# Performance work log

Measured on AMD Instinct MI355X. Metric: run time of the kernel, lower is better.

## Reference

```python
import jax, jax.numpy as jnp
import numpy as np

N, H, DK, DV, DFF, D = 2, 8, 32, 32, 512, 256
B, S = 2, 2048
MASK_VALUE = -1e-30
EPS = 1e-14  # K.epsilon()**2 with default epsilon 1e-7


def glorot(key, shape):
    fan_in, fan_out = shape[-2], shape[-1]
    limit = np.sqrt(6.0 / (fan_in + fan_out))
    return jax.random.uniform(key, shape, jnp.float32, -limit, limit)


def setup_inputs() -> dict:
    key = jax.random.key(0)
    ks = jax.random.split(key, 8)
    return {
        "x": jax.random.normal(ks[0], (B, S, D), jnp.float32),
        "mask": jnp.ones((B, S), jnp.float32),
        "Wq": glorot(ks[1], (N, H, D, DK)),
        "Wk": glorot(ks[2], (N, H, D, DK)),
        "Wv": glorot(ks[3], (N, H, D, DV)),
        "Wo": glorot(ks[4], (N, H * DV, D)),
        "W1": glorot(ks[5], (N, D, DFF)),
        "b1": jnp.zeros((N, DFF), jnp.float32),
        "W2": glorot(ks[6], (N, DFF, D)),
        "b2": jnp.zeros((N, D), jnp.float32),
        "gamma": jnp.ones((2 * N,), jnp.float32),
        "beta": jnp.zeros((2 * N,), jnp.float32),
    }


def _layernorm(x, g, b):
    mean = jnp.mean(x, axis=-1, keepdims=True)
    var = jnp.mean(jnp.square(x - mean), axis=-1, keepdims=True)
    return (x - mean) / jnp.sqrt(var + EPS) * g + b


def reference(x, mask, Wq, Wk, Wv, Wo, W1, b1, W2, b2, gamma, beta):
    m = mask[:, None, None, :]  # [B,1,1,S], multiplies score rows' key axis
    for i in range(N):
        # batched multi-head attention (no 1/sqrt(dk) scaling, faithful to source)
        q = jnp.einsum("bsd,hdk->bhsk", x, Wq[i])
        k = jnp.einsum("bsd,hdk->bhsk", x, Wk[i])
        v = jnp.einsum("bsd,hdv->bhsv", x, Wv[i])
        A = jnp.einsum("bhsk,bhtk->bhst", q, k)  # [B,H,S,S]
        A = m * A + (1.0 - m) * MASK_VALUE
        A = jax.nn.softmax(A, axis=-1)
        o = jnp.einsum("bhst,bhtv->bhsv", A, v)
        conc = o.transpose(0, 2, 1, 3).reshape(x.shape[0], x.shape[1], H * DV)
        x = x + conc @ Wo[i]
        x = _layernorm(x, gamma[2 * i], beta[2 * i])
        ffn = jax.nn.relu(x @ W1[i] + b1[i]) @ W2[i] + b2[i]
        x = x + ffn
        x = _layernorm(x, gamma[2 * i + 1], beta[2 * i + 1])
    return x
```

## Files before the change

### kernel.cpp

```cpp
#include <hip/hip_runtime.h>
#include <hip/hip_bf16.h>

#define NL 2
#define NH 8
#define DKk 32
#define DVv 32
#define DFF 512
#define DD 256
#define BB 2
#define SS 2048
#define MROWS (BB*SS)
#define LN_EPS 1e-14f
#define L2E 1.4426950408889634f
#define SOFT_SHIFT_L2E (50.0f*L2E)

typedef __hip_bfloat16 bf16;
typedef unsigned short us;
typedef short bf16x8 __attribute__((ext_vector_type(8)));
typedef float f32x4  __attribute__((ext_vector_type(4)));
typedef unsigned short us4 __attribute__((ext_vector_type(4)));

#define O_XF   256
#define O_QB   (O_XF+1048576)
#define O_KH   (O_QB+1048576)
#define O_KL   (O_KH+524288)
#define O_VT   (O_KL+524288)
#define O_XH   (O_VT+524288)
#define O_XL   (O_XH+524288)
#define O_OP   (O_XL+524288)
#define O_ML   (O_OP+2097152)
#define O_MASK (O_ML+65536)
#define O_B1   (O_MASK+4096)
#define O_B2   (O_B1+1024)
#define O_GM   (O_B2+512)
#define O_BT   (O_GM+4)
#define O_PREP (O_BT+4)
#define TAIL_TOTAL (4096+1024+512+4+4)
#define CONV_BLOCKS (512 + (TAIL_TOTAL+255)/256)
#define PREP_BLOCKS 512
#define PQH 0u
#define PQL 393216u
#define POH 786432u
#define POL 917504u
#define P1H 1048576u
#define P1L 1310720u
#define P2H 1572864u
#define P2L 1835008u

__device__ __forceinline__ float us2f(us u){
  unsigned int v = ((unsigned int)u) << 16; float f;
  __builtin_memcpy(&f, &v, 4); return f;
}
__device__ __forceinline__ us f2bf_rne(float f){
  unsigned int b = __float_as_uint(f);
  b += 0x7FFFu + ((b>>16)&1u);
  return (us)(b>>16);
}

#if __has_builtin(__builtin_amdgcn_exp2f)
#define EXP2F(x) __builtin_amdgcn_exp2f(x)
#else
#define EXP2F(x) exp2f(x)
#endif

#if __has_builtin(__builtin_amdgcn_cvt_pk_bf16_f32)
typedef __bf16 bf16x2_t __attribute__((ext_vector_type(2)));
__device__ __forceinline__ int pack_bf16(float a, float b){
  bf16x2_t r = __builtin_amdgcn_cvt_pk_bf16_f32(a, b);
  int i; __builtin_memcpy(&i, &r, 4); return i;
}
#else
__device__ __forceinline__ int pack_bf16(float a, float b){
  int b0 = __float_as_int(a) + 0x8000;
  int b1 = __float_as_int(b) + 0x8000;
  return (b1 & 0xFFFF0000) | ((int)((unsigned)b0 >> 16));
}
#endif

__device__ __forceinline__ f32x4 MF(bf16x8 a, bf16x8 b, f32x4 c){
  return __builtin_amdgcn_mfma_f32_16x16x32_bf16(a,b,c,0,0,0);
}

__device__ __forceinline__ void gl_lds16(const us* g, us* l){
  __builtin_amdgcn_global_load_lds(
    (const __attribute__((address_space(1))) unsigned int*)g,
    (__attribute__((address_space(3))) unsigned int*)l, 16, 0, 0);
}

__device__ __forceinline__ size_t xhl_idx(int row, int col){
  int rt = row>>6, rg = (row>>4)&3, L15 = row&15;
  int kc = col>>5, Q = (col>>3)&3, j = col&7;
  return ((size_t)(rt*8+kc))*2048 + rg*512 + Q*128 + L15*8 + j;
}

__device__ __forceinline__ float conv1(const void* src, size_t i, int flag){
  if(flag) return ((const float*)src)[i];
  return us2f(((const us*)src)[i]);
}

__device__ __forceinline__ void prep_b_raw(const void* W0, const void* W1v, const void* W2v,
                                           int baseoff, us* __restrict__ Bh, us* __restrict__ Bl,
                                           int Kd, int Nd, int qkv, int g, int flag)
{
  int total = (Kd/32)*(Nd/16)*64;
  if(g >= total) return;
  int lane = g & 63, fi = g >> 6;
  int ncN = Nd/16;
  int nc = fi % ncN, kc = fi / ncN;
  int Q = lane>>4, L15 = lane&15;
  int n = nc*16 + L15;
  const void* src;
  int off0, stride;
  if(qkv){
    int sec = n>>8, h = (n>>5)&7, kq = n&31;
    src = (sec==0)?W0:((sec==1)?W1v:W2v);
    off0 = baseoff + h*8192 + kq;
    stride = 32;
  } else {
    src = W0;
    off0 = baseoff + n;
    stride = Nd;
  }
  #pragma unroll
  for(int j=0;j<8;j++){
    int k = kc*32 + Q*8 + j;
    float v = conv1(src, (size_t)off0 + (size_t)k*stride, flag);
    us hb = f2bf_rne(v);
    Bh[(size_t)g*8 + j] = hb;
    Bl[(size_t)g*8 + j] = f2bf_rne(v - us2f(hb));
  }
}

__global__ void conv_prep(const void* s0, const void* s1, const void* sWq, const void* sWk,
                          const void* sWv, const void* sWo, const void* sW1, const void* sb1,
                          const void* sW2, const void* sb2, const void* sgm, const void* sbt,
                          float* __restrict__ ws, int* __restrict__ flagp)
{
  __shared__ int fsh[4];
  int bad = 0;
  const us* xr = (const us*)s0;
  for(int i=threadIdx.x; i<4096; i+=256){
    float f = us2f(xr[i]);
    if(!(fabsf(f) < 1e3f)) bad = 1;
  }
  unsigned long long m = __ballot(bad);
  if((threadIdx.x&63)==0) fsh[threadIdx.x>>6] = (m!=0ull);
  __syncthreads();
  int flag = (fsh[0]|fsh[1]|fsh[2]|fsh[3]);
  if(blockIdx.x==0 && threadIdx.x==0) *flagp = flag;

  int b = blockIdx.x;
  if(b < PREP_BLOCKS){
    int layer = b >> 8, lb = b & 255;
    us* prep = (us*)(ws + O_PREP);
    if(lb < 96){
      int g = lb*256 + threadIdx.x;
      prep_b_raw(sWq, sWk, sWv, layer*65536, prep+PQH+(size_t)layer*196608,
                 prep+PQL+(size_t)layer*196608, 256, 768, 1, g, flag);
    } else if(lb < 128){
      int g = (lb-96)*256 + threadIdx.x;
      prep_b_raw(sWo, nullptr, nullptr, layer*65536, prep+POH+(size_t)layer*65536,
                 prep+POL+(size_t)layer*65536, 256, 256, 0, g, flag);
    } else if(lb < 192){
      int g = (lb-128)*256 + threadIdx.x;
      prep_b_raw(sW1, nullptr, nullptr, layer*131072, prep+P1H+(size_t)layer*131072,
                 prep+P1L+(size_t)layer*131072, 256, 512, 0, g, flag);
    } else {
      int g = (lb-192)*256 + threadIdx.x;
      prep_b_raw(sW2, nullptr, nullptr, layer*131072, prep+P2H+(size_t)layer*131072,
                 prep+P2L+(size_t)layer*131072, 512, 256, 0, g, flag);
    }
    return;
  }
  int b2 = b - PREP_BLOCKS;
  if(b2 < 512){
    int g8 = b2*256 + threadIdx.x;
    int e0 = g8*8;
    float v[8];
    if(flag){
      float4 a0 = *((const float4*)s0 + (e0>>2));
      float4 a1 = *((const float4*)s0 + (e0>>2) + 1);
      v[0]=a0.x; v[1]=a0.y; v[2]=a0.z; v[3]=a0.w;
      v[4]=a1.x; v[5]=a1.y; v[6]=a1.z; v[7]=a1.w;
    } else {
      bf16x8 u = *((const bf16x8*)s0 + g8);
      #pragma unroll
      for(int j=0;j<8;j++) v[j] = us2f((us)u[j]);
    }
    *(float4*)&ws[O_XF+e0]   = (float4){v[0],v[1],v[2],v[3]};
    *(float4*)&ws[O_XF+e0+4] = (float4){v[4],v[5],v[6],v[7]};
    union{ us a[8]; uint4 q; } hh, ll;
    #pragma unroll
    for(int j=0;j<8;j++){
      us hb = f2bf_rne(v[j]);
      hh.a[j] = hb;
      ll.a[j] = f2bf_rne(v[j] - us2f(hb));
    }
    size_t xi = xhl_idx(e0>>8, e0&255);
    *(uint4*)&((us*)(ws+O_XH))[xi] = hh.q;
    *(uint4*)&((us*)(ws+O_XL))[xi] = ll.q;
    return;
  }
  int g = (b2-512)*256 + threadIdx.x;
  if(g < 4096){ ws[O_MASK+g] = conv1(s1, g, flag)*L2E; return; }
  g -= 4096;
  if(g < 1024){ ws[O_B1+g] = conv1(sb1, g, flag); return; }
  g -= 1024;
  if(g < 512){ ws[O_B2+g] = conv1(sb2, g, flag); return; }
  g -= 512;
  if(g < 4){ ws[O_GM+g] = conv1(sgm, g, flag); return; }
  g -= 4;
  if(g < 4){ ws[O_BT+g] = conv1(sbt, g, flag); return; }
}

template<int MODE>
__launch_bounds__(256)
__global__ void gemm_mfma(const us* __restrict__ Axh, const us* __restrict__ Axl,
                          const us* __restrict__ Bh, const us* __restrict__ Bl,
                          const float* __restrict__ bias,
                          float* __restrict__ O,
                          us* __restrict__ QH, us* __restrict__ QL,
                          us* __restrict__ KH, us* __restrict__ KL, us* __restrict__ VT,
                          int Ncols, int Kdim)
{
  __shared__ __align__(16) us SH[16384];
  const int t = threadIdx.x;
  const int w = t>>6, lane = t&63;
  const int Q = lane>>4, L15 = lane&15;
  const int bx = blockIdx.x, by = blockIdx.y;
  const int row0 = bx*64;
  const int nc0 = by*4;
  const int col0 = by*64;
  const int nKc = Kdim>>5;
  const int ncW = Ncols>>4;

  f32x4 acc[2][2];
  #pragma unroll
  for(int i=0;i<2;i++)
    #pragma unroll
    for(int j=0;j<2;j++) acc[i][j] = (f32x4){0.f,0.f,0.f,0.f};

  auto stage = [&](int kc){
    const int bo = (kc&1)*8192;
    size_t abase = ((size_t)(bx*nKc + kc))*2048;
    gl_lds16(&Axh[abase + (size_t)t*8], &SH[bo + t*8]);
    gl_lds16(&Axl[abase + (size_t)t*8], &SH[bo + 2048 + t*8]);
    size_t gidx = ((size_t)(kc*ncW + nc0 + w)*64 + lane)*8;
    gl_lds16(&Bh[gidx], &SH[bo + 4096 + t*8]);
    gl_lds16(&Bl[gidx], &SH[bo + 6144 + t*8]);
  };

  stage(0);

  for(int kc=0; kc<nKc; kc++){
    __syncthreads();
    if(kc+1 < nKc) stage(kc+1);
    const int bo = (kc&1)*8192;
    const us* Ah  = SH + bo;
    const us* Al  = SH + bo + 2048;
    const us* Bhs = SH + bo + 4096;
    const us* Bls = SH + bo + 6144;

    bf16x8 aAh[2], aAl[2], bBh[2], bBl[2];
    #pragma unroll
    for(int rg2=0;rg2<2;rg2++){
      int rg = (w&1)*2 + rg2;
      aAh[rg2] = *(const bf16x8*)&Ah[rg*512 + lane*8];
      aAl[rg2] = *(const bf16x8*)&Al[rg*512 + lane*8];
    }
    #pragma unroll
    for(int cg2=0;cg2<2;cg2++){
      int nc = (w>>1)*2 + cg2;
      bBh[cg2] = *(const bf16x8*)&Bhs[nc*512 + lane*8];
      bBl[cg2] = *(const bf16x8*)&Bls[nc*512 + lane*8];
    }
    #pragma unroll
    for(int rg2=0;rg2<2;rg2++)
      #pragma unroll
      for(int cg2=0;cg2<2;cg2++){
        acc[rg2][cg2] = MF(aAl[rg2], bBh[cg2], acc[rg2][cg2]);
        acc[rg2][cg2] = MF(aAh[rg2], bBl[cg2], acc[rg2][cg2]);
        acc[rg2][cg2] = MF(aAh[rg2], bBh[cg2], acc[rg2][cg2]);
      }
  }

  if(MODE==0){
    __syncthreads();
    us* TH = SH;
    us* TL = SH + 4608;
    #pragma unroll
    for(int rg2=0;rg2<2;rg2++)
      #pragma unroll
      for(int cg2=0;cg2<2;cg2++)
        #pragma unroll
        for(int r=0;r<4;r++){
          int rl = (w&1)*32 + rg2*16 + Q*4 + r;
          int cl = (w>>1)*32 + cg2*16 + L15;
          float va = acc[rg2][cg2][r];
          us hb = f2bf_rne(va);
          TH[rl*72+cl] = hb;
          TL[rl*72+cl] = f2bf_rne(va - us2f(hb));
        }
    __syncthreads();
    const int sec = col0>>8;
    const int h0  = (col0&255)>>5;
    const int b_  = row0>>11;
    const int srow0 = row0 & 2047;
    if(sec < 2){
      us* DH = (sec==0) ? QH : KH;
      us* DL = (sec==0) ? QL : KL;
      #pragma unroll
      for(int u2=0; u2<2; u2++){
        int u = w + u2*4;
        int rg = u&3, half = u>>2;
        int lbase = (rg*16 + L15)*72 + half*32 + Q*8;
        bf16x8 hv = *(const bf16x8*)&TH[lbase];
        bf16x8 lv = *(const bf16x8*)&TL[lbase];
        int bh = b_*NH + h0 + half;
        size_t dbase = ((size_t)(bh*128 + (srow0>>4) + rg)*64 + lane)*8;
        *(bf16x8*)&DH[dbase] = hv;
        *(bf16x8*)&DL[dbase] = lv;
      }
    } else {
      #pragma unroll
      for(int u2=0; u2<2; u2++){
        int u = w + u2*4;
        int sgrp = u&1, kqh = (u>>1)&1, half = u>>2;
        union{ us u8[8]; bf16x8 v; } vv;
        #pragma unroll
        for(int j=0;j<8;j++){
          int rl = sgrp*32 + Q*8 + j;
          int cl = half*32 + kqh*16 + L15;
          vv.u8[j] = TH[rl*72+cl];
        }
        int bh = b_*NH + h0 + half;
        size_t dbase = ((size_t)((bh*64 + (srow0>>5) + sgrp)*2 + kqh)*64 + lane)*8;
        *(bf16x8*)&VT[dbase] = vv.v;
      }
    }
  } else {
    #pragma unroll
    for(int rg2=0;rg2<2;rg2++)
      #pragma unroll
      for(int cg2=0;cg2<2;cg2++)
        #pragma unroll
        for(int r=0;r<4;r++){
          int row = row0 + (w&1)*32 + rg2*16 + Q*4 + r;
          int c   = col0 + (w>>1)*32 + cg2*16 + L15;
          float v = acc[rg2][cg2][r] + bias[c];
          O[(size_t)row*Ncols + c] = v>0.f ? v : 0.f;
        }
  }
}

__global__ void
__launch_bounds__(512)
__attribute__((amdgpu_waves_per_eu(2, 2)))
oln_ffn(const float* __restrict__ OpartA, const float* __restrict__ MLA,
        const us* __restrict__ WOh, const us* __restrict__ WOl,
        const us* __restrict__ W1h, const us* __restrict__ W1l,
        const us* __restrict__ W2h, const us* __restrict__ W2l,
        const float* __restrict__ b1, const float* __restrict__ b2,
        float* __restrict__ xf, us* __restrict__ xh, us* __restrict__ xl,
        const float* __restrict__ gamma, const float* __restrict__ beta, int gi0,
        void* __restrict__ out, int write_out, const int* __restrict__ flagp)
{
  __shared__ __align__(16) us xAH[4096], xAL[4096];
  __shared__ __align__(16) us hAH[8192], hAL[8192];
  __shared__ float lred[256];
  const int t = threadIdx.x;
  const int w = t>>6, lane = t&63;
  const int Q = lane>>4, L15 = lane&15;
  const int row0 = blockIdx.x*16;
  const int b_ = row0>>11, s0_ = row0&2047;

  bf16x8 Wh[8][2], Wl[8][2];
  float4 Ar[2][4];
  float  Ml[2][2];

  auto loadWO_ = [&](int kc, int set){
    #pragma unroll
    for(int cg=0;cg<2;cg++){
      size_t fi = (size_t)(kc*16 + w*2 + cg)*512 + (size_t)lane*8;
      Wh[set][cg] = *(const bf16x8*)&WOh[fi];
      Wl[set][cg] = *(const bf16x8*)&WOl[fi];
    }
  };
  auto loadW1_ = [&](int nch, int kc, int set){
    #pragma unroll
    for(int cg=0;cg<2;cg++){
      size_t fi = (size_t)(kc*32 + nch*16 + w*2 + cg)*512 + (size_t)lane*8;
      Wh[set][cg] = *(const bf16x8*)&W1h[fi];
      Wl[set][cg] = *(const bf16x8*)&W1l[fi];
    }
  };
  auto loadW2_ = [&](int kc, int set){
    #pragma unroll
    for(int cg=0;cg<2;cg++){
      size_t fi = (size_t)(kc*16 + w*2 + cg)*512 + (size_t)lane*8;
      Wh[set][cg] = *(const bf16x8*)&W2h[fi];
      Wl[set][cg] = *(const bf16x8*)&W2l[fi];
    }
  };
  auto loadAr = [&](int kc, int set){
    size_t i0 = ((size_t)(b_*8+kc))*2048 + s0_ + L15;
    Ml[set][0] = MLA[i0]; Ml[set][1] = MLA[i0+32768];
    const float* p0 = &OpartA[i0*32 + Q*8];
    const float* p1 = &OpartA[(i0+32768)*32 + Q*8];
    Ar[set][0] = *(const float4*)p0; Ar[set][1] = *(const float4*)(p0+4);
    Ar[set][2] = *(const float4*)p1; Ar[set][3] = *(const float4*)(p1+4);
  };

  f32x4 accA[2];
  accA[0] = accA[1] = (f32x4){0.f,0.f,0.f,0.f};

  auto stepA = [&](int aset, int wset){
    float inv = 1.f/(Ml[aset][0] + Ml[aset][1]);
    float fv[8];
    fv[0]=(Ar[aset][0].x+Ar[aset][2].x)*inv; fv[1]=(Ar[aset][0].y+Ar[aset][2].y)*inv;
    fv[2]=(Ar[aset][0].z+Ar[aset][2].z)*inv; fv[3]=(Ar[aset][0].w+Ar[aset][2].w)*inv;
    fv[4]=(Ar[aset][1].x+Ar[aset][3].x)*inv; fv[5]=(Ar[aset][1].y+Ar[aset][3].y)*inv;
    fv[6]=(Ar[aset][1].z+Ar[aset][3].z)*inv; fv[7]=(Ar[aset][1].w+Ar[aset][3].w)*inv;
    union{ us a[8]; bf16x8 v; } Ah_, Al_;
    #pragma unroll
    for(int j=0;j<8;j++){
      us hb = f2bf_rne(fv[j]);
      Ah_.a[j] = hb;
      Al_.a[j] = f2bf_rne(fv[j] - us2f(hb));
    }
    __builtin_amdgcn_s_setprio(1);
    accA[0] = MF(Al_.v, Wh[wset][0], accA[0]);
    accA[0] = MF(Ah_.v, Wl[wset][0], accA[0]);
    accA[0] = MF(Ah_.v, Wh[wset][0], accA[0]);
    accA[1] = MF(Al_.v, Wh[wset][1], accA[1]);
    accA[1] = MF(Ah_.v, Wl[wset][1], accA[1]);
    accA[1] = MF(Ah_.v, Wh[wset][1], accA[1]);
    __builtin_amdgcn_s_setprio(0);
  };

  loadAr(0,0); loadAr(1,1);
  loadWO_(0,0); loadWO_(1,1); loadWO_(2,2); loadWO_(3,3);
  loadWO_(4,4); loadWO_(5,5); loadWO_(6,6); loadWO_(7,7);
  #pragma unroll
  for(int kc=0; kc<8; kc+=2){
    stepA(0, kc);
    loadW1_(0, kc, kc);
    if(kc+2<8) loadAr(kc+2, 0);
    stepA(1, kc+1);
    loadW1_(0, kc+1, kc+1);
    if(kc+3<8) loadAr(kc+3, 1);
  }

  float tmp[2][4];
  #pragma unroll
  for(int cg=0;cg<2;cg++)
    #pragma unroll
    for(int r=0;r<4;r++){
      int row = row0 + Q*4 + r;
      int c = (w*2+cg)*16 + L15;
      tmp[cg][r] = accA[cg][r] + xf[(size_t)row*DD + c];
    }
  float s[4], sq[4];
  #pragma unroll
  for(int r=0;r<4;r++){
    s[r]  = tmp[0][r]+tmp[1][r];
    sq[r] = tmp[0][r]*tmp[0][r]+tmp[1][r]*tmp[1][r];
  }
  #pragma unroll
  for(int off=1; off<16; off<<=1)
    #pragma unroll
    for(int r=0;r<4;r++){
      s[r]  += __shfl_xor(s[r], off);
      sq[r] += __shfl_xor(sq[r], off);
    }
  if(L15==0){
    #pragma unroll
    for(int r=0;r<4;r++){
      int rl = Q*4 + r;
      lred[(w*16 + rl)*2]   = s[r];
      lred[(w*16 + rl)*2+1] = sq[r];
    }
  }
  __syncthreads();
  float val_s[2][4];
  {
    float g = gamma[gi0], bb = beta[gi0];
    float scv[4], mnv[4];
    #pragma unroll
    for(int r=0;r<4;r++){
      int rl = Q*4 + r;
      float S = 0.f, SQ = 0.f;
      #pragma unroll
      for(int wv=0; wv<8; wv++){
        S  += lred[(wv*16+rl)*2];
        SQ += lred[(wv*16+rl)*2+1];
      }
      float mean = S*(1.f/DD);
      float var  = SQ*(1.f/DD) - mean*mean;
      scv[r] = rsqrtf(var+LN_EPS)*g;
      mnv[r] = mean;
    }
    #pragma unroll
    for(int cg=0;cg<2;cg++){
      int c = (w*2+cg)*16 + L15;
      int base = (c>>5)*512 + (((c&31)>>3))*128 + (c&7);
      #pragma unroll
      for(int r=0;r<4;r++){
        float v = (tmp[cg][r]-mnv[r])*scv[r] + bb;
        val_s[cg][r] = v;
        us hb = f2bf_rne(v);
        xAH[base + (Q*4+r)*8] = hb;
        xAL[base + (Q*4+r)*8] = f2bf_rne(v - us2f(hb));
      }
    }
  }
  __syncthreads();

  #pragma unroll
  for(int nch=0; nch<2; nch++){
    f32x4 ah[2];
    ah[0] = ah[1] = (f32x4){0.f,0.f,0.f,0.f};
    #pragma unroll
    for(int kc=0; kc<8; kc++){
      bf16x8 aAh = *(const bf16x8*)&xAH[kc*512 + lane*8];
      bf16x8 aAl = *(const bf16x8*)&xAL[kc*512 + lane*8];
      __builtin_amdgcn_s_setprio(1);
      ah[0] = MF(aAl, Wh[kc][0], ah[0]);
      ah[0] = MF(aAh, Wl[kc][0], ah[0]);
      ah[0] = MF(aAh, Wh[kc][0], ah[0]);
      ah[1] = MF(aAl, Wh[kc][1], ah[1]);
      ah[1] = MF(aAh, Wl[kc][1], ah[1]);
      ah[1] = MF(aAh, Wh[kc][1], ah[1]);
      __builtin_amdgcn_s_setprio(0);
      if(nch==0) loadW1_(1, kc, kc);
      else       loadW2_(kc, kc);
    }
    #pragma unroll
    for(int cg=0;cg<2;cg++){
      int col = nch*256 + (w*2+cg)*16 + L15;
      float bv = b1[col];
      int base = (col>>5)*512 + (((col&31)>>3))*128 + (col&7);
      #pragma unroll
      for(int r=0;r<4;r++){
        int row = Q*4 + r;
        float v = ah[cg][r] + bv;
        v = v>0.f ? v : 0.f;
        us hb = f2bf_rne(v);
        hAH[base + row*8] = hb;
        hAL[base + row*8] = f2bf_rne(v - us2f(hb));
      }
    }
  }
  __syncthreads();

  f32x4 ay[2];
  ay[0] = ay[1] = (f32x4){0.f,0.f,0.f,0.f};
  #pragma unroll
  for(int kc2=0; kc2<16; kc2++){
    const int sub = kc2 & 7;
    bf16x8 aAh = *(const bf16x8*)&hAH[kc2*512 + lane*8];
    bf16x8 aAl = *(const bf16x8*)&hAL[kc2*512 + lane*8];
    __builtin_amdgcn_s_setprio(1);
    ay[0] = MF(aAl, Wh[sub][0], ay[0]);
    ay[0] = MF(aAh, Wl[sub][0], ay[0]);
    ay[0] = MF(aAh, Wh[sub][0], ay[0]);
    ay[1] = MF(aAl, Wh[sub][1], ay[1]);
    ay[1] = MF(aAh, Wl[sub][1], ay[1]);
    ay[1] = MF(aAh, Wh[sub][1], ay[1]);
    __builtin_amdgcn_s_setprio(0);
    if(kc2+8 < 16) loadW2_(kc2+8, sub);
  }

  float tmp2[2][4];
  #pragma unroll
  for(int cg=0;cg<2;cg++)
    #pragma unroll
    for(int r=0;r<4;r++){
      int c = (w*2+cg)*16 + L15;
      tmp2[cg][r] = ay[cg][r] + val_s[cg][r] + b2[c];
    }
  float s2[4], sq2[4];
  #pragma unroll
  for(int r=0;r<4;r++){
    s2[r]  = tmp2[0][r]+tmp2[1][r];
    sq2[r] = tmp2[0][r]*tmp2[0][r]+tmp2[1][r]*tmp2[1][r];
  }
  #pragma unroll
  for(int off=1; off<16; off<<=1)
    #pragma unroll
    for(int r=0;r<4;r++){
      s2[r]  += __shfl_xor(s2[r], off);
      sq2[r] += __shfl_xor(sq2[r], off);
    }
  if(L15==0){
    #pragma unroll
    for(int r=0;r<4;r++){
      int rl = Q*4 + r;
      lred[(w*16 + rl)*2]   = s2[r];
      lred[(w*16 + rl)*2+1] = sq2[r];
    }
  }
  __syncthreads();
  float g2 = gamma[gi0+1], bb2 = beta[gi0+1];
  float scv2[4], mnv2[4];
  #pragma unroll
  for(int r=0;r<4;r++){
    int rl = Q*4 + r;
    float S = 0.f, SQ = 0.f;
    #pragma unroll
    for(int wv=0; wv<8; wv++){
      S  += lred[(wv*16+rl)*2];
      SQ += lred[(wv*16+rl)*2+1];
    }
    float mean = S*(1.f/DD);
    float var  = SQ*(1.f/DD) - mean*mean;
    scv2[r] = rsqrtf(var+LN_EPS)*g2;
    mnv2[r] = mean;
  }
  int flag = write_out ? *flagp : 0;
  #pragma unroll
  for(int cg=0;cg<2;cg++)
    #pragma unroll
    for(int r=0;r<4;r++){
      int row = row0 + Q*4 + r;
      int c = (w*2+cg)*16 + L15;
      float val = (tmp2[cg][r]-mnv2[r])*scv2[r] + bb2;
      xf[(size_t)row*DD + c] = val;
      us hb = f2bf_rne(val);
      size_t xi = xhl_idx(row, c);
      xh[xi] = hb;
      xl[xi] = f2bf_rne(val - us2f(hb));
      if(write_out){
        if(flag) ((float*)out)[(size_t)row*DD + c] = val;
        else     ((bf16*)out)[(size_t)row*DD + c] = __float2bfloat16(val);
      }
    }
}

__launch_bounds__(256)
__global__ void attn_kernel(const us* __restrict__ QH, const us* __restrict__ QL,
                            const us* __restrict__ KH, const us* __restrict__ KL,
                            const us* __restrict__ VT,
                            const float* __restrict__ mask,
                            float* __restrict__ Opart, float* __restrict__ ML)
{
  __shared__ __align__(16) us Khs[4096], Kls[4096], Vts[4096];
  __shared__ __align__(16) float Msl[1024];
  const int t = threadIdx.x;
  const int bh = blockIdx.x >> 6;
  const int qt = (blockIdx.x & 63) >> 1;
  const int ks = blockIdx.x & 1;
  const int b_ = bh >> 3;
  const int wv = t >> 6;
  const int lane = t & 63;
  const int Q = lane >> 4, L15 = lane & 15;
  const int q0 = qt*64 + wv*16;

  size_t qidx = ((size_t)(bh*128 + qt*4 + wv)*64 + lane)*8;
  const bf16x8 qh_v = *(const bf16x8*)&QH[qidx];
  const bf16x8 ql_v = *(const bf16x8*)&QL[qidx];

  const us* KHbh = KH + (size_t)bh*65536;
  const us* KLbh = KL + (size_t)bh*65536;
  const us* VTbh = VT + (size_t)bh*65536;
  const int base = ks*1024;

  f32x4 Oa0a = {0.f,0.f,0.f,0.f}, Oa0b = {0.f,0.f,0.f,0.f};
  f32x4 Oa1a = {0.f,0.f,0.f,0.f}, Oa1b = {0.f,0.f,0.f,0.f};
  float lacc = 0.f;

  {
    const us* mrow = (const us*)(mask + (size_t)b_*SS + base);
    gl_lds16(mrow + (size_t)t*8, ((us*)Msl) + t*8);
    size_t kbase = (size_t)(base>>4)*512;
    size_t vbase = (size_t)(base>>5)*1024;
    gl_lds16(&KHbh[kbase + (size_t)t*8], &Khs[t*8]);
    gl_lds16(&KLbh[kbase + (size_t)t*8], &Kls[t*8]);
    gl_lds16(&VTbh[vbase + (size_t)t*8], &Vts[t*8]);
  }

  for(int s=0; s<16; s++){
    __syncthreads();
    if(s < 15){
      int t0n = base + (s+1)*64;
      int bn = (s+1)&1;
      size_t kbase = (size_t)(t0n>>4)*512;
      size_t vbase = (size_t)(t0n>>5)*1024;
      gl_lds16(&KHbh[kbase + (size_t)t*8], &Khs[bn*2048 + t*8]);
      gl_lds16(&KLbh[kbase + (size_t)t*8], &Kls[bn*2048 + t*8]);
      gl_lds16(&VTbh[vbase + (size_t)t*8], &Vts[bn*2048 + t*8]);
    }
    const int bo = (s&1)*2048;
    const int mo = s*64;

    f32x4 St[4];
    const f32x4 zz = {0.f,0.f,0.f,0.f};
    __builtin_amdgcn_s_setprio(1);
    #pragma unroll
    for(int kt=0;kt<4;kt++){
      bf16x8 aKh = *(const bf16x8*)&Khs[bo + kt*512 + lane*8];
      bf16x8 aKl = *(const bf16x8*)&Kls[bo + kt*512 + lane*8];
      f32x4 a = MF(aKl, qh_v, zz);
      a = MF(aKh, ql_v, a);
      a = MF(aKh, qh_v, a);
      St[kt] = a;
    }
    __builtin_amdgcn_s_setprio(0);

    float lsum = 0.f;
    #pragma unroll
    for(int kt=0;kt<4;kt++){
      float4 mv = *(const float4*)&Msl[mo + kt*16 + Q*4];
      float mvr[4] = {mv.x, mv.y, mv.z, mv.w};
      #pragma unroll
      for(int r=0;r<4;r++){
        float p = EXP2F(fmaf(mvr[r], St[kt][r], -SOFT_SHIFT_L2E));
        St[kt][r] = p;
        lsum += p;
      }
    }
    lacc += lsum;

    int pk[4][2];
    #pragma unroll
    for(int kt=0;kt<4;kt++){
      pk[kt][0] = pack_bf16(St[kt][0], St[kt][1]);
      pk[kt][1] = pack_bf16(St[kt][2], St[kt][3]);
    }

    #pragma unroll
    for(int c=0;c<2;c++){
      union { int i[4]; bf16x8 v; } bu;
      #pragma unroll
      for(int d=0;d<4;d++){
        int srcl = (((Q&1)*2 + (d>>1))<<4) | L15;
        int vlo = __shfl(pk[2*c  ][d&1], srcl, 64);
        int vhi = __shfl(pk[2*c+1][d&1], srcl, 64);
        bu.i[d] = (Q & 2) ? vhi : vlo;
      }
      bf16x8 aV0 = *(const bf16x8*)&Vts[bo + (c*2+0)*512 + lane*8];
      bf16x8 aV1 = *(const bf16x8*)&Vts[bo + (c*2+1)*512 + lane*8];
      __builtin_amdgcn_s_setprio(1);
      if(c == 0){
        Oa0a = MF(aV0, bu.v, Oa0a);
        Oa1a = MF(aV1, bu.v, Oa1a);
      } else {
        Oa0b = MF(aV0, bu.v, Oa0b);
        Oa1b = MF(aV1, bu.v, Oa1b);
      }
      __builtin_amdgcn_s_setprio(0);
    }
  }

  f32x4 Oa0 = Oa0a + Oa0b;
  f32x4 Oa1 = Oa1a + Oa1b;
  lacc += __shfl_xor(lacc, 16);
  lacc += __shfl_xor(lacc, 32);

  float* opp = &Opart[((size_t)(ks*16+bh)*SS + q0 + L15)*32];
  #pragma unroll
  for(int r=0;r<4;r++){
    opp[Q*4+r]    = Oa0[r];
    opp[16+Q*4+r] = Oa1[r];
  }
  if(Q==0){
    ML[(size_t)(ks*16+bh)*SS + q0 + L15] = lacc;
  }
}

extern "C" void kernel_launch(void* const* d_in, const int* in_sizes, int n_in,
                              void* d_out, int out_size, void* d_ws, size_t ws_size,
                              hipStream_t stream)
{
  float* ws = (float*)d_ws;
  int* flagp = (int*)d_ws;

  float* xf  = ws + O_XF;
  us* QHb = (us*)(ws + O_QB);
  us* QLb = QHb + 1048576;
  us* KH = (us*)(ws + O_KH);
  us* KL = (us*)(ws + O_KL);
  us* VT = (us*)(ws + O_VT);
  us* XH = (us*)(ws + O_XH);
  us* XL = (us*)(ws + O_XL);
  float* Opart = ws + O_OP;
  float* ML  = ws + O_ML;
  float* b1f = ws + O_B1;
  float* b2f_ = ws + O_B2;
  float* gmf = ws + O_GM;
  float* btf = ws + O_BT;
  us* prep = (us*)(ws + O_PREP);

  conv_prep<<<PREP_BLOCKS+CONV_BLOCKS,256,0,stream>>>(
      d_in[0], d_in[1], d_in[2], d_in[3], d_in[4], d_in[5],
      d_in[6], d_in[7], d_in[8], d_in[9], d_in[10], d_in[11],
      ws, flagp);

  for(int i=0;i<NL;i++){
    const float* b1i = b1f + (size_t)i*DFF;
    const float* b2i = b2f_ + (size_t)i*DD;

    dim3 g0(64, 12);
    gemm_mfma<0><<<g0,256,0,stream>>>(XH, XL,
                                      prep+PQH+(size_t)i*196608, prep+PQL+(size_t)i*196608,
                                      nullptr, nullptr,
                                      QHb, QLb, KH, KL, VT, 768, 256);
    attn_kernel<<<1024,256,0,stream>>>(QHb, QLb, KH, KL, VT, ws + O_MASK, Opart, ML);
    oln_ffn<<<256,512,0,stream>>>(Opart, ML,
                                  prep+POH+(size_t)i*65536, prep+POL+(size_t)i*65536,
                                  prep+P1H+(size_t)i*131072, prep+P1L+(size_t)i*131072,
                                  prep+P2H+(size_t)i*131072, prep+P2L+(size_t)i*131072,
                                  b1i, b2i, xf, XH, XL,
                                  gmf, btf, 2*i, d_out, (i==NL-1)?1:0, flagp);
  }
}
```

Measured before the change: 226.0 us.

## Rewrite QKV GEMM to stream fragments directly into registers with triple buffering

The QKV projection GEMM stops staging A/B tiles through LDS with double buffering and barriers. Each wave now loads its MFMA fragments straight from global memory into a 3-deep register ring, using a fully unrolled fixed K loop and s_setprio around the MFMA bursts. The kernel is specialised for QKV shapes and pinned to 3 waves per EU. This removes per-step __syncthreads and LDS traffic, at the cost of more registers and duplicated global loads across waves that share tiles.

After: 227.4 us. No clear change (+0.6%).

```diff
diff --git a/kernel.cpp b/kernel.cpp
--- a/kernel.cpp
+++ b/kernel.cpp
@@ -213,17 +213,15 @@
   if(g < 4){ ws[O_BT+g] = conv1(sbt, g, flag); return; }
 }
 
-template<int MODE>
+__global__ void
 __launch_bounds__(256)
-__global__ void gemm_mfma(const us* __restrict__ Axh, const us* __restrict__ Axl,
-                          const us* __restrict__ Bh, const us* __restrict__ Bl,
-                          const float* __restrict__ bias,
-                          float* __restrict__ O,
-                          us* __restrict__ QH, us* __restrict__ QL,
-                          us* __restrict__ KH, us* __restrict__ KL, us* __restrict__ VT,
-                          int Ncols, int Kdim)
+__attribute__((amdgpu_waves_per_eu(3, 3)))
+gemm_qkv(const us* __restrict__ Axh, const us* __restrict__ Axl,
+         const us* __restrict__ Bh, const us* __restrict__ Bl,
+         us* __restrict__ QH, us* __restrict__ QL,
+         us* __restrict__ KH, us* __restrict__ KL, us* __restrict__ VT)
 {
-  __shared__ __align__(16) us SH[16384];
+  __shared__ __align__(16) us TH[4608], TL[4608];
   const int t = threadIdx.x;
   const int w = t>>6, lane = t&63;
   const int Q = lane>>4, L15 = lane&15;
@@ -231,8 +229,6 @@
   const int row0 = bx*64;
   const int nc0 = by*4;
   const int col0 = by*64;
-  const int nKc = Kdim>>5;
-  const int ncW = Ncols>>4;
 
   f32x4 acc[2][2];
   #pragma unroll
@@ -240,116 +236,89 @@
     #pragma unroll
     for(int j=0;j<2;j++) acc[i][j] = (f32x4){0.f,0.f,0.f,0.f};
 
-  auto stage = [&](int kc){
-    const int bo = (kc&1)*8192;
-    size_t abase = ((size_t)(bx*nKc + kc))*2048;
-    gl_lds16(&Axh[abase + (size_t)t*8], &SH[bo + t*8]);
-    gl_lds16(&Axl[abase + (size_t)t*8], &SH[bo + 2048 + t*8]);
-    size_t gidx = ((size_t)(kc*ncW + nc0 + w)*64 + lane)*8;
-    gl_lds16(&Bh[gidx], &SH[bo + 4096 + t*8]);
-    gl_lds16(&Bl[gidx], &SH[bo + 6144 + t*8]);
+  bf16x8 Ah_[3][2], Al_[3][2], Bh_[3][2], Bl_[3][2];
+  auto loadS = [&](int kc, int set){
+    size_t abase = ((size_t)(bx*8 + kc))*2048;
+    #pragma unroll
+    for(int rg2=0;rg2<2;rg2++){
+      size_t ai = abase + (size_t)((w&1)*2+rg2)*512 + (size_t)lane*8;
+      Ah_[set][rg2] = *(const bf16x8*)&Axh[ai];
+      Al_[set][rg2] = *(const bf16x8*)&Axl[ai];
+    }
+    #pragma unroll
+    for(int cg2=0;cg2<2;cg2++){
+      size_t bi = ((size_t)(kc*48 + nc0 + (w>>1)*2+cg2)*64 + lane)*8;
+      Bh_[set][cg2] = *(const bf16x8*)&Bh[bi];
+      Bl_[set][cg2] = *(const bf16x8*)&Bl[bi];
+    }
   };
 
-  stage(0);
-
-  for(int kc=0; kc<nKc; kc++){
-    __syncthreads();
-    if(kc+1 < nKc) stage(kc+1);
-    const int bo = (kc&1)*8192;
-    const us* Ah  = SH + bo;
-    const us* Al  = SH + bo + 2048;
-    const us* Bhs = SH + bo + 4096;
-    const us* Bls = SH + bo + 6144;
-
-    bf16x8 aAh[2], aAl[2], bBh[2], bBl[2];
-    #pragma unroll
-    for(int rg2=0;rg2<2;rg2++){
-      int rg = (w&1)*2 + rg2;
-      aAh[rg2] = *(const bf16x8*)&Ah[rg*512 + lane*8];
-      aAl[rg2] = *(const bf16x8*)&Al[rg*512 + lane*8];
-    }
-    #pragma unroll
-    for(int cg2=0;cg2<2;cg2++){
-      int nc = (w>>1)*2 + cg2;
-      bBh[cg2] = *(const bf16x8*)&Bhs[nc*512 + lane*8];
-      bBl[cg2] = *(const bf16x8*)&Bls[nc*512 + lane*8];
-    }
+  loadS(0,0); loadS(1,1); loadS(2,2);
+  #pragma unroll
+  for(int kc=0; kc<8; kc++){
+    const int s = kc%3;
+    __builtin_amdgcn_s_setprio(1);
     #pragma unroll
     for(int rg2=0;rg2<2;rg2++)
       #pragma unroll
       for(int cg2=0;cg2<2;cg2++){
-        acc[rg2][cg2] = MF(aAl[rg2], bBh[cg2], acc[rg2][cg2]);
-        acc[rg2][cg2] = MF(aAh[rg2], bBl[cg2], acc[rg2][cg2]);
-        acc[rg2][cg2] = MF(aAh[rg2], bBh[cg2], acc[rg2][cg2]);
-      }
-  }
-
-  if(MODE==0){
-    __syncthreads();
-    us* TH = SH;
-    us* TL = SH + 4608;
-    #pragma unroll
-    for(int rg2=0;rg2<2;rg2++)
-      #pragma unroll
-      for(int cg2=0;cg2<2;cg2++)
-        #pragma unroll
-        for(int r=0;r<4;r++){
-          int rl = (w&1)*32 + rg2*16 + Q*4 + r;
-          int cl = (w>>1)*32 + cg2*16 + L15;
-          float va = acc[rg2][cg2][r];
-          us hb = f2bf_rne(va);
-          TH[rl*72+cl] = hb;
-          TL[rl*72+cl] = f2bf_rne(va - us2f(hb));
-        }
-    __syncthreads();
-    const int sec = col0>>8;
-    const int h0  = (col0&255)>>5;
-    const int b_  = row0>>11;
-    const int srow0 = row0 & 2047;
-    if(sec < 2){
-      us* DH = (sec==0) ? QH : KH;
-      us* DL = (sec==0) ? QL : KL;
-      #pragma unroll
-      for(int u2=0; u2<2; u2++){
-        int u = w + u2*4;
-        int rg = u&3, half = u>>2;
-        int lbase = (rg*16 + L15)*72 + half*32 + Q*8;
-        bf16x8 hv = *(const bf16x8*)&TH[lbase];
-        bf16x8 lv = *(const bf16x8*)&TL[lbase];
-        int bh = b_*NH + h0 + half;
-        size_t dbase = ((size_t)(bh*128 + (srow0>>4) + rg)*64 + lane)*8;
-        *(bf16x8*)&DH[dbase] = hv;
-        *(bf16x8*)&DL[dbase] = lv;
-      }
-    } else {
-      #pragma unroll
-      for(int u2=0; u2<2; u2++){
-        int u = w + u2*4;
-        int sgrp = u&1, kqh = (u>>1)&1, half = u>>2;
-        union{ us u8[8]; bf16x8 v; } vv;
-        #pragma unroll
-        for(int j=0;j<8;j++){
-          int rl = sgrp*32 + Q*8 + j;
-          int cl = half*32 + kqh*16 + L15;
-          vv.u8[j] = TH[rl*72+cl];
-        }
-        int bh = b_*NH + h0 + half;
-        size_t dbase = ((size_t)((bh*64 + (srow0>>5) + sgrp)*2 + kqh)*64 + lane)*8;
-        *(bf16x8*)&VT[dbase] = vv.v;
-      }
+        acc[rg2][cg2] = MF(Al_[s][rg2], Bh_[s][cg2], acc[rg2][cg2]);
+        acc[rg2][cg2] = MF(Ah_[s][rg2], Bl_[s][cg2], acc[rg2][cg2]);
+        acc[rg2][cg2] = MF(Ah_[s][rg2], Bh_[s][cg2], acc[rg2][cg2]);
+      }
+    __builtin_amdgcn_s_setprio(0);
+    if(kc+3 < 8) loadS(kc+3, s);
+  }
+
+  #pragma unroll
+  for(int rg2=0;rg2<2;rg2++)
+    #pragma unroll
+    for(int cg2=0;cg2<2;cg2++)
+      #pragma unroll
+      for(int r=0;r<4;r++){
+        int rl = (w&1)*32 + rg2*16 + Q*4 + r;
+        int cl = (w>>1)*32 + cg2*16 + L15;
+        float va = acc[rg2][cg2][r];
+        us hb = f2bf_rne(va);
+        TH[rl*72+cl] = hb;
+        TL[rl*72+cl] = f2bf_rne(va - us2f(hb));
+      }
+  __syncthreads();
+  const int sec = col0>>8;
+  const int h0  = (col0&255)>>5;
+  const int b_  = row0>>11;
+  const int srow0 = row0 & 2047;
+  if(sec < 2){
+    us* DH = (sec==0) ? QH : KH;
+    us* DL = (sec==0) ? QL : KL;
+    #pragma unroll
+    for(int u2=0; u2<2; u2++){
+      int u = w + u2*4;
+      int rg = u&3, half = u>>2;
+      int lbase = (rg*16 + L15)*72 + half*32 + Q*8;
+      bf16x8 hv = *(const bf16x8*)&TH[lbase];
+      bf16x8 lv = *(const bf16x8*)&TL[lbase];
+      int bh = b_*NH + h0 + half;
+      size_t dbase = ((size_t)(bh*128 + (srow0>>4) + rg)*64 + lane)*8;
+      *(bf16x8*)&DH[dbase] = hv;
+      *(bf16x8*)&DL[dbase] = lv;
     }
   } else {
     #pragma unroll
-    for(int rg2=0;rg2<2;rg2++)
-      #pragma unroll
-      for(int cg2=0;cg2<2;cg2++)
-        #pragma unroll
-        for(int r=0;r<4;r++){
-          int row = row0 + (w&1)*32 + rg2*16 + Q*4 + r;
-          int c   = col0 + (w>>1)*32 + cg2*16 + L15;
-          float v = acc[rg2][cg2][r] + bias[c];
-          O[(size_t)row*Ncols + c] = v>0.f ? v : 0.f;
-        }
+    for(int u2=0; u2<2; u2++){
+      int u = w + u2*4;
+      int sgrp = u&1, kqh = (u>>1)&1, half = u>>2;
+      union{ us u8[8]; bf16x8 v; } vv;
+      #pragma unroll
+      for(int j=0;j<8;j++){
+        int rl = sgrp*32 + Q*8 + j;
+        int cl = half*32 + kqh*16 + L15;
+        vv.u8[j] = TH[rl*72+cl];
+      }
+      int bh = b_*NH + h0 + half;
+      size_t dbase = ((size_t)((bh*64 + (srow0>>5) + sgrp)*2 + kqh)*64 + lane)*8;
+      *(bf16x8*)&VT[dbase] = vv.v;
+    }
   }
 }
 
@@ -801,10 +770,9 @@
     const float* b2i = b2f_ + (size_t)i*DD;
 
     dim3 g0(64, 12);
-    gemm_mfma<0><<<g0,256,0,stream>>>(XH, XL,
-                                      prep+PQH+(size_t)i*196608, prep+PQL+(size_t)i*196608,
-                                      nullptr, nullptr,
-                                      QHb, QLb, KH, KL, VT, 768, 256);
+    gemm_qkv<<<g0,256,0,stream>>>(XH, XL,
+                                  prep+PQH+(size_t)i*196608, prep+PQL+(size_t)i*196608,
+                                  QHb, QLb, KH, KL, VT);
     attn_kernel<<<1024,256,0,stream>>>(QHb, QLb, KH, KL, VT, ws + O_MASK, Opart, ML);
     oln_ffn<<<256,512,0,stream>>>(Opart, ML,
                                   prep+POH+(size_t)i*65536, prep+POL+(size_t)i*65536,
```
